# Kernel optimization log

Measured on AMD Instinct MI355X. Metric: run time of the kernel, lower is better.

## Reference

```python
import jax, jax.numpy as jnp
import numpy as np

NUM_ENTITIES = 100000
BATCH_SIZE = 4096
E_STATIC = 250000
E_NEW = 4096
D_ENT = 128
D_REL = 64
N_REL = 9
N_TYPES = 3
N_INTENTS = 8
NUM_LAYERS = 3
SCALE = 0.05


def _make_edges(key, n):
    ks = jax.random.split(key, 5)
    src = jax.random.randint(ks[0], (n,), 0, NUM_ENTITIES, dtype=jnp.int32)
    st = jax.random.randint(ks[1], (n,), 0, N_TYPES, dtype=jnp.int32)
    tgt = jax.random.randint(ks[2], (n,), 0, NUM_ENTITIES, dtype=jnp.int32)
    tt = jax.random.randint(ks[3], (n,), 0, N_TYPES, dtype=jnp.int32)
    rel = jax.random.randint(ks[4], (n,), 0, N_REL, dtype=jnp.int32)
    return jnp.stack([src, st, tgt, tt, rel], axis=1)


def setup_inputs() -> dict:
    key = jax.random.key(0)
    ks = jax.random.split(key, 16)
    return {
        'new_edges': _make_edges(ks[0], E_NEW),
        'new_node_types': jax.random.randint(ks[1], (BATCH_SIZE,), 0, N_TYPES, dtype=jnp.int32),
        'static_edges': _make_edges(ks[2], E_STATIC),
        'entity_embeddings': SCALE * jax.random.normal(ks[3], (NUM_ENTITIES - BATCH_SIZE, D_ENT), jnp.float32),
        'default_emb': SCALE * jax.random.normal(ks[4], (N_TYPES, D_ENT), jnp.float32),
        'relation_emb': SCALE * jax.random.normal(ks[5], (N_REL, D_REL), jnp.float32),
        'W_rel': SCALE * jax.random.normal(ks[6], (N_REL, D_ENT, D_REL), jnp.float32),
        'b_rel': SCALE * jax.random.normal(ks[7], (N_REL, D_REL), jnp.float32),
        'W_msg': SCALE * jax.random.normal(ks[8], (N_REL, D_ENT, D_ENT), jnp.float32),
        'W_intent': SCALE * jax.random.normal(ks[9], (N_TYPES, D_ENT, N_INTENTS), jnp.float32),
        'b_intent': SCALE * jax.random.normal(ks[10], (N_TYPES, N_INTENTS), jnp.float32),
        'W_ibn': SCALE * jax.random.normal(ks[11], (N_TYPES, N_INTENTS, N_REL), jnp.float32),
        'b_ibn': SCALE * jax.random.normal(ks[12], (N_TYPES, N_REL), jnp.float32),
    }


def multi_dense(lookups, values, W, b=None, act=None):
    # Same math as tf.gather(W, lookups) followed by values @ w, but computed
    # against all D (<=9) weight slices then selected, to avoid materializing
    # a [E, d_in, d_out] gathered-weights tensor.
    out_all = jnp.einsum('ei,dio->edo', values, W)  # [E, D, d_out]
    out = jnp.take_along_axis(out_all, lookups[:, None, None], axis=1)[:, 0]
    if b is not None:
        out = out + b[lookups]
    return act(out) if act is not None else out


def reference(new_edges, new_node_types, static_edges, entity_embeddings,
              default_emb, relation_emb, W_rel, b_rel, W_msg,
              W_intent, b_intent, W_ibn, b_ibn):
    edges = jnp.concatenate([new_edges, static_edges], axis=0)  # [E, 5]
    sources = edges[:, 0]
    targets = edges[:, 2]
    target_types = edges[:, 3]
    relations = edges[:, 4]

    rel_e = relation_emb[relations]  # [E, D_REL]
    # first BATCH_SIZE entity slots come from type default embeddings
    ent = jnp.concatenate([default_emb[new_node_types], entity_embeddings], axis=0)  # [N, D_ENT]

    layer_edge_weights = []
    for _ in range(NUM_LAYERS):
        src = ent[sources]  # [E, D_ENT]
        tgt = ent[targets]  # [E, D_ENT]
        # per-target intent distribution and per-relation intent weights
        intents = multi_dense(target_types, tgt, W_intent, b_intent, jax.nn.softmax)  # [E, N_INTENTS]
        rel_w = multi_dense(target_types, intents, W_ibn, b_ibn, jax.nn.softmax)  # [E, N_REL]
        iw = jnp.take_along_axis(rel_w, relations[:, None], axis=1)[:, 0]  # [E]
        # per-relation transform of source embeddings
        src_rel = multi_dense(relations, src, W_rel, b_rel, jax.nn.selu)  # [E, D_REL]
        scores = jnp.einsum('er,er,e->e', src_rel, rel_e, iw)  # [E]
        exp_s = jnp.exp(scores)
        denom = jax.ops.segment_sum(exp_s, targets, num_segments=NUM_ENTITIES)  # [N]
        # tf.math.reciprocal_no_nan semantics
        safe = jnp.where(denom != 0, denom, 1.0)
        recip = jnp.where(denom != 0, 1.0 / safe, 0.0)
        dist = exp_s * recip[targets]  # scatter-softmax over incoming edges
        # inference: dropout is identity
        msg = dist[:, None] * multi_dense(relations, src, W_msg, None, None)  # [E, D_ENT]
        ent = jax.ops.segment_sum(msg, targets, num_segments=NUM_ENTITIES)  # [N, D_ENT]
        layer_edge_weights.append(dist)

    return ent, jnp.stack(layer_edge_weights)  # [N, D_ENT], [L, E]
```

## Files before the change

kernel.cpp:

```cpp
#include <hip/hip_runtime.h>
#include <cstddef>
#include <cstdint>

#define NE 100000
#define EN 4096
#define ET 254096
#define D 128
#define DR 64
#define NR 9
#define NT 3
#define NI 8
#define TE 256
#define TILES_X 28

using frag  = __attribute__((ext_vector_type(8))) short;
using f32x4 = __attribute__((ext_vector_type(4))) float;
using u32x4 = __attribute__((ext_vector_type(4))) unsigned int;

__device__ __forceinline__ ushort f2b(float x) {
  union { float f; uint32_t u; } v; v.f = x;
  uint32_t r = v.u + 0x7FFFu + ((v.u >> 16) & 1u);
  return (ushort)(r >> 16);
}

__device__ __forceinline__ uint32_t cvtpk(float lo, float hi) {
  uint32_t r;
  asm("v_cvt_pk_bf16_f32 %0, %1, %2" : "=v"(r) : "v"(lo), "v"(hi));
  return r;
}

__device__ __forceinline__ frag lds_rd(const ushort* b, int row, int k) {
  const int ch = ((k >> 3) ^ (row & 7));
  return *(const frag*)(b + row * D + (ch << 3));
}
__device__ __forceinline__ void lds_wr(ushort* b, int row, int ch, frag v) {
  *(frag*)(b + row * D + ((ch ^ (row & 7)) << 3)) = v;
}
__device__ __forceinline__ void lds_wr2(ushort* b, int row, int k, uint32_t v) {
  const int ch = (k >> 3) ^ (row & 7);
  *(uint32_t*)(b + row * D + (ch << 3) + (k & 7)) = v;
}

__global__ void k_init(ushort* __restrict__ entb, const int* __restrict__ ntypes,
                       const float* __restrict__ def, const float* __restrict__ emb) {
  int i = blockIdx.x * blockDim.x + threadIdx.x;
  if (i >= NE * (D / 4)) return;
  int row = i >> 5, ch = i & 31;
  float4 v;
  if (row < EN) v = ((const float4*)(def + ntypes[row] * D))[ch];
  else v = ((const float4*)(emb + (size_t)(row - EN) * D))[ch];
  ushort4 h;
  h.x = f2b(v.x); h.y = f2b(v.y); h.z = f2b(v.z); h.w = f2b(v.w);
  ((ushort4*)entb)[i] = h;
}

__global__ void k_zero_cnt(int* cnt) { if (threadIdx.x < 48) cnt[threadIdx.x] = 0; }

__global__ __launch_bounds__(256) void k_wconv(const float* __restrict__ Wr,
                                               const float* __restrict__ Wm,
                                               ushort* __restrict__ wrelb,
                                               ushort* __restrict__ wmsgb) {
  const int nrel = NR * DR * (D / 8);
  const int nmsg = NR * D * (D / 8);
  int idx = blockIdx.x * 256 + threadIdx.x;
  if (idx < nrel) {
    int r = idx / (DR * 16), rem = idx % (DR * 16), n = rem / 16, sc = rem % 16;
    int kb = (sc ^ (n & 7)) * 8;
    const float* s = Wr + (size_t)r * D * DR + (size_t)kb * DR + n;
    uint4 pk;
    pk.x = cvtpk(s[0 * DR], s[1 * DR]); pk.y = cvtpk(s[2 * DR], s[3 * DR]);
    pk.z = cvtpk(s[4 * DR], s[5 * DR]); pk.w = cvtpk(s[6 * DR], s[7 * DR]);
    *(uint4*)(wrelb + (size_t)r * DR * D + n * D + sc * 8) = pk;
  } else if (idx < nrel + nmsg) {
    int j = idx - nrel;
    int r = j / (D * 16), rem = j % (D * 16), n = rem / 16, sc = rem % 16;
    int kb = (sc ^ (n & 7)) * 8;
    const float* s = Wm + (size_t)r * D * D + (size_t)kb * D + n;
    uint4 pk;
    pk.x = cvtpk(s[0 * D], s[1 * D]); pk.y = cvtpk(s[2 * D], s[3 * D]);
    pk.z = cvtpk(s[4 * D], s[5 * D]); pk.w = cvtpk(s[6 * D], s[7 * D]);
    *(uint4*)(wmsgb + (size_t)r * D * D + n * D + sc * 8) = pk;
  }
}

__global__ __launch_bounds__(256) void k_hist2(const int* __restrict__ nedg,
                                               const int* __restrict__ sedg,
                                               int* __restrict__ cnt,
                                               int* __restrict__ thist) {
  __shared__ int h[NR];
  if (threadIdx.x < NR) h[threadIdx.x] = 0;
  __syncthreads();
  int e = blockIdx.x * 256 + threadIdx.x;
  if (e < ET) {
    const int* p = (e < EN) ? nedg + (size_t)e * 5 : sedg + (size_t)(e - EN) * 5;
    atomicAdd(&h[p[4]], 1);
    atomicAdd(&thist[p[2]], 1);
  }
  __syncthreads();
  if (threadIdx.x < NR && h[threadIdx.x]) atomicAdd(&cnt[threadIdx.x], h[threadIdx.x]);
}

__global__ void k_prefix(const int* __restrict__ cnt, int* __restrict__ base,
                         int* __restrict__ head) {
  if (threadIdx.x == 0) {
    int acc = 0;
    for (int r = 0; r < NR; r++) { base[r] = acc; head[r] = acc; acc += cnt[r]; }
  }
}

__global__ __launch_bounds__(256) void k_scan1(const int* __restrict__ hist,
                                               int* __restrict__ local_ex,
                                               int* __restrict__ bsum, int n) {
  __shared__ int s[256];
  int i = blockIdx.x * 256 + threadIdx.x;
  int v = (i < n) ? hist[i] : 0;
  s[threadIdx.x] = v;
  __syncthreads();
  for (int off = 1; off < 256; off <<= 1) {
    int t = (threadIdx.x >= off) ? s[threadIdx.x - off] : 0;
    __syncthreads();
    s[threadIdx.x] += t;
    __syncthreads();
  }
  if (i < n) local_ex[i] = s[threadIdx.x] - v;
  if (threadIdx.x == 255) bsum[blockIdx.x] = s[255];
}

__global__ __launch_bounds__(512) void k_scan2(int* __restrict__ bsum, int nb) {
  __shared__ int s[512];
  int v = (threadIdx.x < nb) ? bsum[threadIdx.x] : 0;
  s[threadIdx.x] = v;
  __syncthreads();
  for (int off = 1; off < 512; off <<= 1) {
    int t = (threadIdx.x >= off) ? s[threadIdx.x - off] : 0;
    __syncthreads();
    s[threadIdx.x] += t;
    __syncthreads();
  }
  if (threadIdx.x < nb) bsum[threadIdx.x] = s[threadIdx.x] - v;
}

__global__ void k_scan3(int* __restrict__ tgt_off, const int* __restrict__ bsum,
                        int* __restrict__ thead) {
  int i = blockIdx.x * 256 + threadIdx.x;
  if (i < NE) {
    int v = tgt_off[i] + bsum[i >> 8];
    tgt_off[i] = v;
    thead[i] = v;
  }
  if (i == 0) tgt_off[NE] = ET;
}

__global__ __launch_bounds__(256) void k_scatter3(const int* __restrict__ nedg,
                                                  const int* __restrict__ sedg,
                                                  int* __restrict__ head,
                                                  int* __restrict__ thead,
                                                  int4* __restrict__ epack,
                                                  int2* __restrict__ tp2) {
  __shared__ int h[NR], bb[NR];
  if (threadIdx.x < NR) h[threadIdx.x] = 0;
  __syncthreads();
  int e = blockIdx.x * 256 + threadIdx.x;
  int r = -1, pos = 0, s = 0, t = 0, tt = 0;
  if (e < ET) {
    const int* p = (e < EN) ? nedg + (size_t)e * 5 : sedg + (size_t)(e - EN) * 5;
    s = p[0]; t = p[2]; tt = p[3]; r = p[4];
    pos = atomicAdd(&h[r], 1);
  }
  __syncthreads();
  if (threadIdx.x < NR)
    bb[threadIdx.x] = h[threadIdx.x] ? atomicAdd(&head[threadIdx.x], h[threadIdx.x]) : 0;
  __syncthreads();
  if (r >= 0) {
    int pt = atomicAdd(&thead[t], 1);
    epack[bb[r] + pos] = make_int4(s, (t * NT + tt) * NR, pt, 0);
    tp2[e] = make_int2(pt, t);
  }
}

__global__ __launch_bounds__(1024) void k_iw(
    const ushort* __restrict__ entb,
    const float* __restrict__ W_int, const float* __restrict__ b_int,
    const float* __restrict__ W_ibn, const float* __restrict__ b_ibn,
    float* __restrict__ IW) {
  __shared__ ushort sE[256 * D];
  __shared__ ushort sWi[NT * 16 * D];
  __shared__ float sInt3[256 * 25];
  __shared__ float sbint[NT * NI], sWibn[NT * NI * NR], sbibn[NT * NR];

  const int tid = threadIdx.x;
  const int lane = tid & 63, wv = tid >> 6, g = lane >> 4, c = lane & 15;

  {
    float a[2], b[2];
#pragma unroll
    for (int j = 0; j < 2; j++) {
      int i = tid + j * 1024;
      if (i < NT * NI * (D / 2)) {
        int tt = i / (NI * D / 2), rem = i % (NI * D / 2), jj = rem / (D / 2), k2 = rem % (D / 2);
        const float* Wi = W_int + (size_t)tt * D * NI;
        a[j] = Wi[(2 * k2) * NI + jj]; b[j] = Wi[(2 * k2 + 1) * NI + jj];
      }
    }
#pragma unroll
    for (int j = 0; j < 2; j++) {
      int i = tid + j * 1024;
      if (i < NT * NI * (D / 2)) {
        int tt = i / (NI * D / 2), rem = i % (NI * D / 2), jj = rem / (D / 2), k2 = rem % (D / 2);
        lds_wr2(sWi, tt * 16 + jj, 2 * k2, cvtpk(a[j], b[j]));
      }
    }
  }
  for (int i = tid; i < NT * 8 * (D / 2); i += 1024) {
    int tt = i / (8 * D / 2), rem = i % (8 * D / 2), j = rem / (D / 2), k2 = rem % (D / 2);
    lds_wr2(sWi, tt * 16 + 8 + j, 2 * k2, 0u);
  }
  if (tid < NT * NI) sbint[tid] = b_int[tid];
  for (int i = tid; i < NT * NI * NR; i += 1024) sWibn[i] = W_ibn[i];
  if (tid < NT * NR) sbibn[tid] = b_ibn[tid];

  const int ebase = blockIdx.x * 256;
  const int nrow = min(256, NE - ebase);
  {
    frag tmp[4];
#pragma unroll
    for (int j = 0; j < 4; j++) {
      int i = tid + j * 1024, row = i >> 4, ch = i & 15;
      tmp[j] = (row < nrow) ? ((const frag*)(entb + (size_t)(ebase + row) * D))[ch] : (frag){};
    }
#pragma unroll
    for (int j = 0; j < 4; j++) {
      int i = tid + j * 1024, row = i >> 4, ch = i & 15;
      lds_wr(sE, row, ch, tmp[j]);
    }
  }
  __syncthreads();

  {
    f32x4 accI[NT];
#pragma unroll
    for (int tt = 0; tt < NT; tt++) accI[tt] = (f32x4){0.f, 0.f, 0.f, 0.f};
#pragma unroll
    for (int ks = 0; ks < 4; ks++) {
      const int k = ks * 32 + g * 8;
      frag a = lds_rd(sE, wv * 16 + c, k);
#pragma unroll
      for (int tt = 0; tt < NT; tt++) {
        frag b = lds_rd(sWi, tt * 16 + c, k);
        accI[tt] = __builtin_amdgcn_mfma_f32_16x16x32_bf16(a, b, accI[tt], 0, 0, 0);
      }
    }
    if (c < NI) {
      const int rb = wv * 16 + g * 4;
#pragma unroll
      for (int tt = 0; tt < NT; tt++)
#pragma unroll
        for (int q = 0; q < 4; q++) sInt3[(rb + q) * 25 + tt * 8 + c] = accI[tt][q];
    }
  }
  __syncthreads();

  float* stg = (float*)sE;
  {
    const int row = tid & 255, tt = tid >> 8;
    if (tt < NT && row < nrow) {
      float it[NI], mx = -1e30f;
#pragma unroll
      for (int j = 0; j < NI; j++) {
        it[j] = sInt3[row * 25 + tt * 8 + j] + sbint[tt * NI + j];
        mx = fmaxf(mx, it[j]);
      }
      float ssum = 0.f;
#pragma unroll
      for (int j = 0; j < NI; j++) { it[j] = __expf(it[j] - mx); ssum += it[j]; }
      const float inv = 1.f / ssum;
      float qv[NR];
#pragma unroll
      for (int k = 0; k < NR; k++) qv[k] = sbibn[tt * NR + k];
#pragma unroll
      for (int j = 0; j < NI; j++) {
        const float ij = it[j] * inv;
#pragma unroll
        for (int k = 0; k < NR; k++) qv[k] = fmaf(ij, sWibn[(tt * NI + j) * NR + k], qv[k]);
      }
      float m9 = qv[0];
#pragma unroll
      for (int k = 1; k < NR; k++) m9 = fmaxf(m9, qv[k]);
      float s9 = 0.f;
#pragma unroll
      for (int k = 0; k < NR; k++) s9 += __expf(qv[k] - m9);
      const float i9 = 1.f / s9;
#pragma unroll
      for (int k = 0; k < NR; k++) stg[row * 27 + tt * 9 + k] = __expf(qv[k] - m9) * i9;
    }
  }
  __syncthreads();

  const int n27 = nrow * 27;
  float* outp = IW + (size_t)ebase * 27;
  for (int i = tid; i < n27; i += 1024) outp[i] = stg[i];
}

__global__ __launch_bounds__(1024) void k_pass1(
    const ushort* __restrict__ entb,
    const int4* __restrict__ epack,
    const int* __restrict__ cnt, const int* __restrict__ base_g,
    const float* __restrict__ IW,
    const float* __restrict__ rel_emb, const float* __restrict__ b_rel,
    const ushort* __restrict__ wrelb, const ushort* __restrict__ wmsgb,
    ushort* __restrict__ msgbuf, float* __restrict__ exps_b) {
  const int r = blockIdx.y;
  __shared__ ushort sA[TE * D];
  __shared__ ushort sWm[D * D];
  __shared__ ushort sWr[DR * D];
  __shared__ int sTP[TE];
  __shared__ float sIW[TE];
  __shared__ float sbrel[DR], srele[DR];

  const int tid = threadIdx.x;
  const int lane = tid & 63;
  const int wv = tid >> 6;
  const int g = lane >> 4;
  const int c = lane & 15;
  const int row = tid & 255, h = tid >> 8;

  {
    const frag* wr = (const frag*)(wrelb + (size_t)r * DR * D);
    ((frag*)sWr)[tid] = wr[tid];
    const frag* wm = (const frag*)(wmsgb + (size_t)r * D * D);
    ((frag*)sWm)[tid] = wm[tid];
    ((frag*)sWm)[tid + 1024] = wm[tid + 1024];
  }
  if (tid < DR) { sbrel[tid] = b_rel[r * DR + tid]; srele[tid] = rel_emb[r * DR + tid]; }

  const int nr = cnt[r];
  const int bbase = base_g[r];
  const int ntiles = (nr + TE - 1) / TE;

  int4 mp; frag tmp[4]; float iwv = 0.f;
  auto prefetch = [&](int t_) {
    int eidx = t_ * TE + row;
    if (eidx >= nr) eidx = 0;
    mp = epack[bbase + eidx];
    const frag* rp = (const frag*)(entb + (size_t)mp.x * D);
#pragma unroll
    for (int j = 0; j < 4; j++) tmp[j] = rp[h * 4 + j];
    iwv = IW[mp.y + r];
  };

  int tile = blockIdx.x;
  if (tile < ntiles) prefetch(tile);

  for (; tile < ntiles; tile += gridDim.x) {
    const int ne = min(TE, nr - tile * TE);
    __syncthreads();

#pragma unroll
    for (int j = 0; j < 4; j++) lds_wr(sA, row, h * 4 + j, tmp[j]);
    if (h == 0) { sTP[row] = mp.z; sIW[row] = iwv; }
    __syncthreads();

    const int nxt = tile + gridDim.x;
    if (nxt < ntiles) prefetch(nxt);

    f32x4 accR[4], accM[8];
#pragma unroll
    for (int nt = 0; nt < 4; nt++) accR[nt] = (f32x4){0.f, 0.f, 0.f, 0.f};
#pragma unroll
    for (int nt = 0; nt < 8; nt++) accM[nt] = (f32x4){0.f, 0.f, 0.f, 0.f};
#pragma unroll
    for (int ks = 0; ks < 4; ks++) {
      const int k = ks * 32 + g * 8;
      frag a0 = lds_rd(sA, wv * 16 + c, k);
#pragma unroll
      for (int nt = 0; nt < 4; nt++) {
        frag b = lds_rd(sWr, nt * 16 + c, k);
        accR[nt] = __builtin_amdgcn_mfma_f32_16x16x32_bf16(a0, b, accR[nt], 0, 0, 0);
      }
#pragma unroll
      for (int nt = 0; nt < 8; nt++) {
        frag b = lds_rd(sWm, nt * 16 + c, k);
        accM[nt] = __builtin_amdgcn_mfma_f32_16x16x32_bf16(a0, b, accM[nt], 0, 0, 0);
      }
    }

    const int mb = wv * 16 + g * 4;

    float es[4];
    {
      float v[4] = {0.f, 0.f, 0.f, 0.f};
#pragma unroll
      for (int nt = 0; nt < 4; nt++) {
        const int col = nt * 16 + c;
        const float br = sbrel[col], re = srele[col];
#pragma unroll
        for (int q = 0; q < 4; q++) {
          const float x = accR[nt][q] + br;
          const float sl = x > 0.f ? 1.0507009873554805f * x
                                   : 1.7580993408473766f * (__expf(x) - 1.f);
          v[q] = fmaf(sl, re, v[q]);
        }
      }
#pragma unroll
      for (int off = 1; off < 16; off <<= 1)
#pragma unroll
        for (int q = 0; q < 4; q++) v[q] += __shfl_xor(v[q], off, 64);
#pragma unroll
      for (int q = 0; q < 4; q++) {
        const int m = mb + q;
        es[q] = __expf(v[q] * sIW[m]);
        if (c == 0 && m < ne) exps_b[bbase + tile * TE + m] = es[q];
      }
    }

    {
#pragma unroll
      for (int q = 0; q < 4; q++) {
        const int m = mb + q;
        ushort* mrow = msgbuf + (size_t)sTP[m] * D;
#pragma unroll
        for (int nt = 0; nt < 8; nt++) {
          float val = accM[nt][q] * es[q];
          float other = __shfl_xor(val, 1, 64);
          if (!(c & 1) && m < ne)
            *(uint32_t*)(mrow + nt * 16 + c) = cvtpk(val, other);
        }
      }
    }
  }
}

__global__ __launch_bounds__(256) void k_perm(const int4* __restrict__ epack,
                                              const float* __restrict__ exps_b,
                                              float* __restrict__ exps_s) {
  int i = blockIdx.x * 256 + threadIdx.x;
  if (i < ET) exps_s[epack[i].z] = exps_b[i];
}

__global__ __launch_bounds__(256) void k_agg(
    const ushort* __restrict__ msgbuf, const float* __restrict__ exps_s,
    const int* __restrict__ tgt_off,
    ushort* __restrict__ entb, float* __restrict__ fout,
    float* __restrict__ drec, int last) {
  const int lg = threadIdx.x & 15;
  const int grp = threadIdx.x >> 4;
  const int ngrp = gridDim.x * 16;
  for (int t = blockIdx.x * 16 + grp; t < NE; t += ngrp) {
    const int beg = tgt_off[t], end = tgt_off[t + 1];
    float a[8] = {0.f, 0.f, 0.f, 0.f, 0.f, 0.f, 0.f, 0.f};
    float dsum = 0.f;
    for (int j = beg; j < end; j++) {
      const u32x4 pk = __builtin_nontemporal_load((const u32x4*)(msgbuf + (size_t)j * D + lg * 8));
      dsum += exps_s[j];
      a[0] += __uint_as_float(pk.x << 16); a[1] += __uint_as_float(pk.x & 0xFFFF0000u);
      a[2] += __uint_as_float(pk.y << 16); a[3] += __uint_as_float(pk.y & 0xFFFF0000u);
      a[4] += __uint_as_float(pk.z << 16); a[5] += __uint_as_float(pk.z & 0xFFFF0000u);
      a[6] += __uint_as_float(pk.w << 16); a[7] += __uint_as_float(pk.w & 0xFFFF0000u);
    }
    const float rec = (dsum != 0.f) ? 1.f / dsum : 0.f;
    if (lg == 0) drec[t] = rec;
#pragma unroll
    for (int i = 0; i < 8; i++) a[i] *= rec;
    if (last) {
      float4* o = (float4*)(fout + (size_t)t * D + lg * 8);
      o[0] = make_float4(a[0], a[1], a[2], a[3]);
      o[1] = make_float4(a[4], a[5], a[6], a[7]);
    } else {
      uint4 pk;
      pk.x = (uint32_t)f2b(a[0]) | ((uint32_t)f2b(a[1]) << 16);
      pk.y = (uint32_t)f2b(a[2]) | ((uint32_t)f2b(a[3]) << 16);
      pk.z = (uint32_t)f2b(a[4]) | ((uint32_t)f2b(a[5]) << 16);
      pk.w = (uint32_t)f2b(a[6]) | ((uint32_t)f2b(a[7]) << 16);
      *(uint4*)(entb + (size_t)t * D + lg * 8) = pk;
    }
  }
}

__global__ __launch_bounds__(256) void k_dist2(const int2* __restrict__ tp2,
                                               const float* __restrict__ exps_s,
                                               const float* __restrict__ drec,
                                               float* __restrict__ dout) {
  int e = blockIdx.x * 256 + threadIdx.x;
  if (e >= ET) return;
  const int2 v = tp2[e];
  dout[e] = exps_s[v.x] * drec[v.y];
}

extern "C" void kernel_launch(void* const* d_in, const int* in_sizes, int n_in,
                              void* d_out, int out_size, void* d_ws, size_t ws_size,
                              hipStream_t stream) {
  const int* nedg = (const int*)d_in[0];
  const int* ntypes = (const int*)d_in[1];
  const int* sedg = (const int*)d_in[2];
  const float* emb = (const float*)d_in[3];
  const float* def = (const float*)d_in[4];
  const float* rel_emb = (const float*)d_in[5];
  const float* W_rel = (const float*)d_in[6];
  const float* b_rel = (const float*)d_in[7];
  const float* W_msg = (const float*)d_in[8];
  const float* W_int = (const float*)d_in[9];
  const float* b_int = (const float*)d_in[10];
  const float* W_ibn = (const float*)d_in[11];
  const float* b_ibn = (const float*)d_in[12];
  float* out = (float*)d_out;

  char* w = (char*)d_ws;
  size_t off = 0;
  ushort* entb = (ushort*)(w + off); off += (size_t)NE * D * 2;
  ushort* msgbuf = (ushort*)(w + off); off += (size_t)ET * D * 2;
  float* exps_s = (float*)(w + off); off += (size_t)ET * 4;
  float* exps_b = (float*)(w + off); off += (size_t)ET * 4;
  int4* epack = (int4*)(w + off); off += (size_t)ET * 16;
  int2* tp2 = (int2*)(w + off); off += (size_t)ET * 8;
  int* tgt_off = (int*)(w + off); off += (size_t)(NE + 4) * 4;
  int* thead = (int*)(w + off); off += (size_t)NE * 4;
  int* thist = (int*)(w + off); off += (size_t)NE * 4;
  float* drec = (float*)(w + off); off += (size_t)NE * 4;
  int* bsum = (int*)(w + off); off += 2048;
  int* cnt = (int*)(w + off); off += 192;
  float* IW = (float*)(w + off); off += (size_t)NE * NT * NR * 4;
  ushort* wrelb = (ushort*)(w + off); off += (size_t)NR * DR * D * 2;
  ushort* wmsgb = (ushort*)(w + off); off += (size_t)NR * D * D * 2;
  int* base_g = cnt + 16;
  int* head = cnt + 32;
  float* dist_base = out + (size_t)NE * D;

  const int eblocks = (ET + 255) / 256;
  const int nb = (NE + 255) / 256;
  const int wblocks = (NR * DR * (D / 8) + NR * D * (D / 8) + 255) / 256;

  k_init<<<dim3((NE * (D / 4) + 255) / 256), 256, 0, stream>>>(entb, ntypes, def, emb);
  k_zero_cnt<<<1, 64, 0, stream>>>(cnt);
  (void)hipMemsetAsync(thist, 0, (size_t)NE * 4, stream);
  k_wconv<<<dim3(wblocks), 256, 0, stream>>>(W_rel, W_msg, wrelb, wmsgb);
  k_hist2<<<dim3(eblocks), 256, 0, stream>>>(nedg, sedg, cnt, thist);
  k_prefix<<<1, 64, 0, stream>>>(cnt, base_g, head);
  k_scan1<<<dim3(nb), 256, 0, stream>>>(thist, tgt_off, bsum, NE);
  k_scan2<<<1, 512, 0, stream>>>(bsum, nb);
  k_scan3<<<dim3(nb), 256, 0, stream>>>(tgt_off, bsum, thead);
  k_scatter3<<<dim3(eblocks), 256, 0, stream>>>(nedg, sedg, head, thead, epack, tp2);

  for (int l = 0; l < 3; l++) {
    k_iw<<<dim3(nb), 1024, 0, stream>>>(entb, W_int, b_int, W_ibn, b_ibn, IW);
    k_pass1<<<dim3(TILES_X, NR), 1024, 0, stream>>>(
        entb, epack, cnt, base_g, IW, rel_emb, b_rel, wrelb, wmsgb, msgbuf, exps_b);
    k_perm<<<dim3(eblocks), 256, 0, stream>>>(epack, exps_b, exps_s);
    k_agg<<<dim3(2048), 256, 0, stream>>>(msgbuf, exps_s, tgt_off, entb, out, drec, l == 2);
    k_dist2<<<dim3(eblocks), 256, 0, stream>>>(tp2, exps_s, drec,
                                               dist_base + (size_t)l * ET);
  }
}
```

Baseline: 340.3 us.

## Hold relation weights in registers and use 32x32 MFMA in pass1

The pass1 kernel stops staging W_rel and W_msg tiles in shared memory. Each wave now keeps its B-operand fragments in registers and computes with 32x32x16 bf16 MFMA instead of 16x16x32, and the weight conversion drops the XOR swizzle to match. The score reduction is split across two waves and combined through shared memory, which adds an extra barrier. The launch bounds request and TILES_X are raised to allow more blocks. This cuts LDS traffic and frees LDS, in exchange for heavy register pressure from 24 resident fragments plus three 16-wide accumulators.

```diff
diff --git a/kernel.cpp b/kernel.cpp
--- a/kernel.cpp
+++ b/kernel.cpp
@@ -11,11 +11,12 @@
 #define NT 3
 #define NI 8
 #define TE 256
-#define TILES_X 28
-
-using frag  = __attribute__((ext_vector_type(8))) short;
-using f32x4 = __attribute__((ext_vector_type(4))) float;
-using u32x4 = __attribute__((ext_vector_type(4))) unsigned int;
+#define TILES_X 56
+
+using frag   = __attribute__((ext_vector_type(8))) short;
+using f32x4  = __attribute__((ext_vector_type(4))) float;
+using f32x16 = __attribute__((ext_vector_type(16))) float;
+using u32x4  = __attribute__((ext_vector_type(4))) unsigned int;
 
 __device__ __forceinline__ ushort f2b(float x) {
   union { float f; uint32_t u; } v; v.f = x;
@@ -65,8 +66,7 @@
   int idx = blockIdx.x * 256 + threadIdx.x;
   if (idx < nrel) {
     int r = idx / (DR * 16), rem = idx % (DR * 16), n = rem / 16, sc = rem % 16;
-    int kb = (sc ^ (n & 7)) * 8;
-    const float* s = Wr + (size_t)r * D * DR + (size_t)kb * DR + n;
+    const float* s = Wr + (size_t)r * D * DR + (size_t)(sc * 8) * DR + n;
     uint4 pk;
     pk.x = cvtpk(s[0 * DR], s[1 * DR]); pk.y = cvtpk(s[2 * DR], s[3 * DR]);
     pk.z = cvtpk(s[4 * DR], s[5 * DR]); pk.w = cvtpk(s[6 * DR], s[7 * DR]);
@@ -74,8 +74,7 @@
   } else if (idx < nrel + nmsg) {
     int j = idx - nrel;
     int r = j / (D * 16), rem = j % (D * 16), n = rem / 16, sc = rem % 16;
-    int kb = (sc ^ (n & 7)) * 8;
-    const float* s = Wm + (size_t)r * D * D + (size_t)kb * D + n;
+    const float* s = Wm + (size_t)r * D * D + (size_t)(sc * 8) * D + n;
     uint4 pk;
     pk.x = cvtpk(s[0 * D], s[1 * D]); pk.y = cvtpk(s[2 * D], s[3 * D]);
     pk.z = cvtpk(s[4 * D], s[5 * D]); pk.w = cvtpk(s[6 * D], s[7 * D]);
@@ -301,7 +300,7 @@
   for (int i = tid; i < n27; i += 1024) outp[i] = stg[i];
 }
 
-__global__ __launch_bounds__(1024) void k_pass1(
+__global__ __launch_bounds__(1024, 8) void k_pass1(
     const ushort* __restrict__ entb,
     const int4* __restrict__ epack,
     const int* __restrict__ cnt, const int* __restrict__ base_g,
@@ -311,8 +310,8 @@
     ushort* __restrict__ msgbuf, float* __restrict__ exps_b) {
   const int r = blockIdx.y;
   __shared__ ushort sA[TE * D];
-  __shared__ ushort sWm[D * D];
-  __shared__ ushort sWr[DR * D];
+  __shared__ float sPart[2][TE];
+  __shared__ float sES[TE];
   __shared__ int sTP[TE];
   __shared__ float sIW[TE];
   __shared__ float sbrel[DR], srele[DR];
@@ -320,18 +319,26 @@
   const int tid = threadIdx.x;
   const int lane = tid & 63;
   const int wv = tid >> 6;
-  const int g = lane >> 4;
-  const int c = lane & 15;
+  const int mb = wv >> 1;
+  const int ng = wv & 1;
+  const int cl = lane & 31;
+  const int hf = lane >> 5;
   const int row = tid & 255, h = tid >> 8;
 
+  if (tid < DR) { sbrel[tid] = b_rel[r * DR + tid]; srele[tid] = rel_emb[r * DR + tid]; }
+
+  frag bR[8], bM0[8], bM1[8];
   {
-    const frag* wr = (const frag*)(wrelb + (size_t)r * DR * D);
-    ((frag*)sWr)[tid] = wr[tid];
-    const frag* wm = (const frag*)(wmsgb + (size_t)r * D * D);
-    ((frag*)sWm)[tid] = wm[tid];
-    ((frag*)sWm)[tid + 1024] = wm[tid + 1024];
-  }
-  if (tid < DR) { sbrel[tid] = b_rel[r * DR + tid]; srele[tid] = rel_emb[r * DR + tid]; }
+    const ushort* wr = wrelb + (size_t)r * DR * D + (size_t)(ng * 32 + cl) * D + hf * 8;
+    const ushort* wm0 = wmsgb + (size_t)r * D * D + (size_t)(ng * 64 + cl) * D + hf * 8;
+    const ushort* wm1 = wm0 + 32 * D;
+#pragma unroll
+    for (int ks = 0; ks < 8; ks++) {
+      bR[ks] = *(const frag*)(wr + ks * 16);
+      bM0[ks] = *(const frag*)(wm0 + ks * 16);
+      bM1[ks] = *(const frag*)(wm1 + ks * 16);
+    }
+  }
 
   const int nr = cnt[r];
   const int bbase = base_g[r];
@@ -363,67 +370,61 @@
     const int nxt = tile + gridDim.x;
     if (nxt < ntiles) prefetch(nxt);
 
-    f32x4 accR[4], accM[8];
-#pragma unroll
-    for (int nt = 0; nt < 4; nt++) accR[nt] = (f32x4){0.f, 0.f, 0.f, 0.f};
-#pragma unroll
-    for (int nt = 0; nt < 8; nt++) accM[nt] = (f32x4){0.f, 0.f, 0.f, 0.f};
-#pragma unroll
-    for (int ks = 0; ks < 4; ks++) {
-      const int k = ks * 32 + g * 8;
-      frag a0 = lds_rd(sA, wv * 16 + c, k);
-#pragma unroll
-      for (int nt = 0; nt < 4; nt++) {
-        frag b = lds_rd(sWr, nt * 16 + c, k);
-        accR[nt] = __builtin_amdgcn_mfma_f32_16x16x32_bf16(a0, b, accR[nt], 0, 0, 0);
-      }
-#pragma unroll
-      for (int nt = 0; nt < 8; nt++) {
-        frag b = lds_rd(sWm, nt * 16 + c, k);
-        accM[nt] = __builtin_amdgcn_mfma_f32_16x16x32_bf16(a0, b, accM[nt], 0, 0, 0);
-      }
-    }
-
-    const int mb = wv * 16 + g * 4;
-
-    float es[4];
+    f32x16 accR = {}, accM0 = {}, accM1 = {};
+#pragma unroll
+    for (int ks = 0; ks < 8; ks++) {
+      frag a = lds_rd(sA, mb * 32 + cl, ks * 16 + hf * 8);
+      accR = __builtin_amdgcn_mfma_f32_32x32x16_bf16(a, bR[ks], accR, 0, 0, 0);
+      accM0 = __builtin_amdgcn_mfma_f32_32x32x16_bf16(a, bM0[ks], accM0, 0, 0, 0);
+      accM1 = __builtin_amdgcn_mfma_f32_32x32x16_bf16(a, bM1[ks], accM1, 0, 0, 0);
+    }
+
     {
-      float v[4] = {0.f, 0.f, 0.f, 0.f};
-#pragma unroll
-      for (int nt = 0; nt < 4; nt++) {
-        const int col = nt * 16 + c;
-        const float br = sbrel[col], re = srele[col];
-#pragma unroll
-        for (int q = 0; q < 4; q++) {
-          const float x = accR[nt][q] + br;
-          const float sl = x > 0.f ? 1.0507009873554805f * x
-                                   : 1.7580993408473766f * (__expf(x) - 1.f);
-          v[q] = fmaf(sl, re, v[q]);
+      const int col = ng * 32 + cl;
+      const float br = sbrel[col], re = srele[col];
+      float v[16];
+#pragma unroll
+      for (int reg = 0; reg < 16; reg++) {
+        const float x = accR[reg] + br;
+        const float sl = x > 0.f ? 1.0507009873554805f * x
+                                 : 1.7580993408473766f * (__expf(x) - 1.f);
+        v[reg] = sl * re;
+      }
+#pragma unroll
+      for (int off = 1; off < 32; off <<= 1)
+#pragma unroll
+        for (int reg = 0; reg < 16; reg++) v[reg] += __shfl_xor(v[reg], off, 64);
+      if (cl == 0) {
+#pragma unroll
+        for (int reg = 0; reg < 16; reg++) {
+          const int rw = mb * 32 + (reg & 3) + 8 * (reg >> 2) + 4 * hf;
+          sPart[ng][rw] = v[reg];
         }
       }
-#pragma unroll
-      for (int off = 1; off < 16; off <<= 1)
-#pragma unroll
-        for (int q = 0; q < 4; q++) v[q] += __shfl_xor(v[q], off, 64);
-#pragma unroll
-      for (int q = 0; q < 4; q++) {
-        const int m = mb + q;
-        es[q] = __expf(v[q] * sIW[m]);
-        if (c == 0 && m < ne) exps_b[bbase + tile * TE + m] = es[q];
-      }
-    }
+    }
+    __syncthreads();
+
+    if (tid < TE) {
+      const float es = __expf((sPart[0][tid] + sPart[1][tid]) * sIW[tid]);
+      sES[tid] = es;
+      if (tid < ne) exps_b[bbase + tile * TE + tid] = es;
+    }
+    __syncthreads();
 
     {
 #pragma unroll
-      for (int q = 0; q < 4; q++) {
-        const int m = mb + q;
-        ushort* mrow = msgbuf + (size_t)sTP[m] * D;
-#pragma unroll
-        for (int nt = 0; nt < 8; nt++) {
-          float val = accM[nt][q] * es[q];
-          float other = __shfl_xor(val, 1, 64);
-          if (!(c & 1) && m < ne)
-            *(uint32_t*)(mrow + nt * 16 + c) = cvtpk(val, other);
+      for (int reg = 0; reg < 16; reg++) {
+        const int rw = mb * 32 + (reg & 3) + 8 * (reg >> 2) + 4 * hf;
+        const float es = sES[rw];
+        ushort* mrow = msgbuf + (size_t)sTP[rw] * D;
+        const int col = ng * 64 + cl;
+        float v0 = accM0[reg] * es;
+        float o0 = __shfl_xor(v0, 1, 64);
+        float v1 = accM1[reg] * es;
+        float o1 = __shfl_xor(v1, 1, 64);
+        if (!(cl & 1) && rw < ne) {
+          *(uint32_t*)(mrow + col) = cvtpk(v0, o0);
+          *(uint32_t*)(mrow + col + 32) = cvtpk(v1, o1);
         }
       }
     }
```

New measurement: 1.149 ms. 238% more time.
